# Kernel tuning notes

Hardware: AMD Instinct MI355X
Metric: run time of the kernel (lower is better)

The kernel has to match this reference:

```python
import jax, jax.numpy as jnp
import numpy as np

N_NODES = 50000
N_EDGES = 800000
D_FEAT = 64
K_HOPS = 8


def setup_inputs() -> dict:
    key = jax.random.key(0)
    k1, k2 = jax.random.split(key)
    feature = jax.random.normal(k1, (N_NODES, D_FEAT), dtype=jnp.float32)
    edge_index = jax.random.randint(k2, (2, N_EDGES), 0, N_NODES, dtype=jnp.int32)
    return {"feature": feature, "edge_index": edge_index}


def reference(feature, edge_index):
    # with A_hat = D^{-1/2} (A + I) D^{-1/2} (add_remaining_self_loops + sym_norm).
    n = feature.shape[0]
    src, dst = edge_index[0], edge_index[1]
    # add_remaining_self_loops: drop any existing self-loop edges (weight -> 0)
    # and append a self loop of weight fill_value=1 for every node. Zeroing the
    # weight is mathematically identical to removing the edge.
    ew = jnp.where(src == dst, 0.0, 1.0).astype(feature.dtype)
    loop = jnp.arange(n, dtype=src.dtype)
    row = jnp.concatenate([src, loop])          # message source (x_j)
    col = jnp.concatenate([dst, loop])          # aggregation target (i)
    w = jnp.concatenate([ew, jnp.ones((n,), dtype=feature.dtype)])
    # symmetric normalization: deg over row, norm = d^-1/2[row] * w * d^-1/2[col]
    deg = jax.ops.segment_sum(w, row, num_segments=n)
    deg_inv_sqrt = jnp.where(deg > 0, jax.lax.rsqrt(deg), 0.0)
    norm = deg_inv_sqrt[row] * w * deg_inv_sqrt[col]  # [E+N]

    xs = [feature]
    x = feature
    for _ in range(K_HOPS):  # small fixed K, structural loop
        # gather-scale-scatter_add: out[i] = sum_{(j,i) in E} norm * x[j]
        x = jax.ops.segment_sum(norm[:, None] * x[row], col, num_segments=n)
        xs.append(x)
    return jnp.concatenate(xs, axis=1)  # [N, (K+1)*D]
```

## Files before the change

### kernel.cpp

```cpp
#include <hip/hip_runtime.h>
#include <hip/hip_fp16.h>
#include <hip/hip_fp8.h>

#define N_NODES 50000
#define N_EDGES 800000
#define D_FEAT 64
#define K_HOPS 8
#define OUT_STRIDE ((K_HOPS + 1) * D_FEAT)
#define NPART 128
#define CHUNK (N_EDGES / NPART)
#define NWORD (N_NODES / 2)

#define SCAN_WORDS 512
#define SCAN_NB ((NWORD + SCAN_WORDS - 1) / SCAN_WORDS)

#define NOCT (N_NODES / 8)

#define ALIGN256(x) (((x) + 255) & ~(size_t)255)
static const size_t OFF_P     = 0;
static const size_t OFF_BASES = OFF_P + (size_t)NPART * NWORD * 4;
static const size_t OFF_OFF   = ALIGN256(OFF_BASES + (size_t)NPART * N_NODES * 4);
static const size_t OFF_BSUM  = ALIGN256(OFF_OFF   + (size_t)(N_NODES + 1) * 4);
static const size_t OFF_TOTW  = ALIGN256(OFF_BSUM  + 64 * 4);
static const size_t OFF_DINV  = ALIGN256(OFF_TOTW  + (size_t)NWORD * 4);
static const size_t OFF_CSR   = ALIGN256(OFF_DINV  + (size_t)N_NODES * 4);
static const size_t OFF_XA    = ALIGN256(OFF_CSR   + (size_t)N_EDGES * 4);
static const size_t OFF_XB    = ALIGN256(OFF_XA + (size_t)(N_NODES + 1) * D_FEAT);

__device__ __forceinline__ float2 fp8x2_to_f2(unsigned short s) {
    __hip_fp8x2_e4m3 v;
    v.__x = (__hip_fp8x2_storage_t)s;
    return (float2)v;
}
__device__ __forceinline__ unsigned short f2_to_fp8x2(float a, float b) {
    __hip_fp8x2_e4m3 v(make_float2(a, b));
    return (unsigned short)v.__x;
}
__device__ __forceinline__ unsigned pack_fp8x4(float a, float b, float c, float d) {
    return (unsigned)f2_to_fp8x2(a, b) | ((unsigned)f2_to_fp8x2(c, d) << 16);
}


__global__ __launch_bounds__(256, 1) void k_hist(const int* __restrict__ src,
                                                 const int* __restrict__ dst,
                                                 unsigned* __restrict__ p) {
    __shared__ unsigned h[NWORD];
    int t = threadIdx.x;
    int base = blockIdx.x * CHUNK;
    for (int w = t; w < NWORD; w += 256) h[w] = 0u;
    __syncthreads();
    for (int j = t; j < CHUNK; j += 256) {
        int s = src[base + j], d = dst[base + j];
        if (s != d) {
            atomicAdd(&h[s >> 1], 1u << (8 * (s & 1)));
            atomicAdd(&h[d >> 1], 65536u << (8 * (d & 1)));
        }
    }
    __syncthreads();
    unsigned* o = p + (size_t)blockIdx.x * NWORD;
    for (int w = t; w < NWORD; w += 256) o[w] = h[w];
}

__global__ void k_sum(const unsigned* __restrict__ p, float* __restrict__ dinv,
                      unsigned* __restrict__ totW) {
    int w = blockIdx.x * blockDim.x + threadIdx.x;
    if (w >= NWORD) return;
    unsigned s0 = 0, s1 = 0, s2 = 0, s3 = 0;
    #pragma unroll 4
    for (int c = 0; c < NPART; c += 4) {
        s0 += p[(size_t)(c + 0) * NWORD + w];
        s1 += p[(size_t)(c + 1) * NWORD + w];
        s2 += p[(size_t)(c + 2) * NWORD + w];
        s3 += p[(size_t)(c + 3) * NWORD + w];
    }
    unsigned s = (s0 + s1) + (s2 + s3);
    dinv[2 * w + 0] = rsqrtf((float)((s & 0xffu) + 1u));
    dinv[2 * w + 1] = rsqrtf((float)(((s >> 8) & 0xffu) + 1u));
    totW[w] = ((s >> 16) & 0xffu) | ((s >> 24) << 16);
}

__global__ void k_scan_sums(const unsigned* __restrict__ totW, int* __restrict__ bsum) {
    __shared__ int lds[256];
    int b = blockIdx.x, t = threadIdx.x;
    int wend = min((b + 1) * SCAN_WORDS, NWORD);
    int tot = 0;
    for (int w = b * SCAN_WORDS + t; w < wend; w += 256) {
        unsigned v = totW[w];
        tot += (int)(v & 0xffffu) + (int)(v >> 16);
    }
    lds[t] = tot; __syncthreads();
    for (int str = 128; str > 0; str >>= 1) {
        if (t < str) lds[t] += lds[t + str];
        __syncthreads();
    }
    if (t == 0) bsum[b] = lds[0];
}

__global__ void k_scan_top(int* __restrict__ bsum) {
    int lane = threadIdx.x;
    int orig = (lane < SCAN_NB) ? bsum[lane] : 0;
    int v = orig;
    for (int d = 1; d < 64; d <<= 1) {
        int u = __shfl_up(v, d, 64);
        if (lane >= d) v += u;
    }
    if (lane < SCAN_NB) bsum[lane] = v - orig;
}

__global__ void k_scan_downA(const unsigned* __restrict__ totW, const int* __restrict__ bsum,
                             int* __restrict__ off) {
    __shared__ int lds[256];
    int b = blockIdx.x, t = threadIdx.x;
    int w0 = b * SCAN_WORDS + 2 * t;
    unsigned t0 = (w0 < NWORD) ? totW[w0] : 0u;
    unsigned t1 = (w0 + 1 < NWORD) ? totW[w0 + 1] : 0u;
    int n[4] = { (int)(t0 & 0xffffu), (int)(t0 >> 16),
                 (int)(t1 & 0xffffu), (int)(t1 >> 16) };
    int tsum = (n[0] + n[1]) + (n[2] + n[3]);
    lds[t] = tsum; __syncthreads();
    int x = tsum;
    for (int d = 1; d < 256; d <<= 1) {
        int u = (t >= d) ? lds[t - d] : 0;
        __syncthreads();
        x += u;
        lds[t] = x;
        __syncthreads();
    }
    int pfx = (x - tsum) + bsum[b];
    #pragma unroll
    for (int j = 0; j < 4; ++j) {
        int node = 2 * w0 + j;
        if (node < N_NODES) {
            off[node] = pfx;
            pfx += n[j];
        } else if (node == N_NODES) {
            off[node] = pfx;
        }
    }
}

__global__ void k_bases(const unsigned* __restrict__ p, const int* __restrict__ off,
                        int* __restrict__ bases) {
    int node = blockIdx.x * blockDim.x + threadIdx.x;
    if (node >= N_NODES) return;
    int w = node >> 1;
    int sh = 16 + 8 * (node & 1);
    int acc = off[node];
    for (int c = 0; c < NPART; ++c) {
        bases[(size_t)c * N_NODES + node] = acc;
        acc += (int)((p[(size_t)c * NWORD + w] >> sh) & 0xffu);
    }
}

__global__ __launch_bounds__(256, 1) void k_scatter(const int* __restrict__ src,
                                                    const int* __restrict__ dst,
                                                    const int* __restrict__ bases,
                                                    int* __restrict__ csr) {
    __shared__ unsigned h[NWORD];
    int t = threadIdx.x;
    int base = blockIdx.x * CHUNK;
    const int* bp = bases + (size_t)blockIdx.x * N_NODES;
    for (int w = t; w < NWORD; w += 256) h[w] = 0u;
    __syncthreads();
    for (int j = t; j < CHUNK; j += 256) {
        int s = src[base + j], d = dst[base + j];
        if (s == d) continue;
        unsigned old = atomicAdd(&h[d >> 1], (d & 1) ? 65536u : 1u);
        unsigned pw = (d & 1) ? (old >> 16) : (old & 0xffffu);
        csr[bp[d] + (int)pw] = s;
    }
}


__global__ void k_x0(const float4* __restrict__ feat4, float4* __restrict__ out4,
                     unsigned* __restrict__ y8, const float* __restrict__ dinv) {
    int t = blockIdx.x * blockDim.x + threadIdx.x;
    if (t >= (N_NODES + 1) * 16) return;
    int row = t >> 4;
    if (row < N_NODES) {
        float4 v = feat4[t];
        out4[(size_t)row * (OUT_STRIDE / 4) + (t & 15)] = v;
        float di = dinv[row];
        y8[t] = pack_fp8x4(v.x * di, v.y * di, v.z * di, v.w * di);
    } else {
        y8[t] = 0u;
    }
}

template <bool WRITE_HALF>
__global__ __launch_bounds__(256) void k_hopf8(
    const uint2* __restrict__ yin,
    float4* __restrict__ outcol4,
    uint2* __restrict__ yout,
    const int* __restrict__ off, const int* __restrict__ csr,
    const float* __restrict__ dinv) {
    int ow = (blockIdx.x * blockDim.x + threadIdx.x) >> 6;
    if (ow >= NOCT) return;
    int lane = threadIdx.x & 63;
    int f = lane & 7;
    int node = ow * 8 + (lane >> 3);
    int e0 = off[node], e1 = off[node + 1];
    int deg = e1 - e0;
    float di = dinv[node];
    float a0 = 0.f, a1 = 0.f, a2 = 0.f, a3 = 0.f;
    float a4 = 0.f, a5 = 0.f, a6 = 0.f, a7 = 0.f;
    {
        uint2 sv = yin[(size_t)node * 8 + f];
        float2 u;
        u = fp8x2_to_f2((unsigned short)(sv.x & 0xffffu)); a0 = u.x; a1 = u.y;
        u = fp8x2_to_f2((unsigned short)(sv.x >> 16));     a2 = u.x; a3 = u.y;
        u = fp8x2_to_f2((unsigned short)(sv.y & 0xffffu)); a4 = u.x; a5 = u.y;
        u = fp8x2_to_f2((unsigned short)(sv.y >> 16));     a6 = u.x; a7 = u.y;
    }

    int nm = deg;
    #pragma unroll
    for (int d = 32; d; d >>= 1) nm = max(nm, __shfl_xor(nm, d, 64));

    int gbase = lane & ~7;

    #define ACC8(q)                                                        \
        {                                                                  \
            float2 u_;                                                     \
            u_ = fp8x2_to_f2((unsigned short)((q).x & 0xffffu));           \
            a0 += u_.x; a1 += u_.y;                                        \
            u_ = fp8x2_to_f2((unsigned short)((q).x >> 16));               \
            a2 += u_.x; a3 += u_.y;                                        \
            u_ = fp8x2_to_f2((unsigned short)((q).y & 0xffffu));           \
            a4 += u_.x; a5 += u_.y;                                        \
            u_ = fp8x2_to_f2((unsigned short)((q).y >> 16));               \
            a6 += u_.x; a7 += u_.y;                                        \
        }

    int cvec = csr[min(e0 + f, N_EDGES - 1)];
    for (int j = 0; j < nm; j += 8) {
        int cnext = csr[min(e0 + j + 8 + f, N_EDGES - 1)];
        int v0 = (j + 0 < deg) ? __shfl(cvec, gbase + 0, 64) : N_NODES;
        int v1 = (j + 1 < deg) ? __shfl(cvec, gbase + 1, 64) : N_NODES;
        int v2 = (j + 2 < deg) ? __shfl(cvec, gbase + 2, 64) : N_NODES;
        int v3 = (j + 3 < deg) ? __shfl(cvec, gbase + 3, 64) : N_NODES;
        int v4 = (j + 4 < deg) ? __shfl(cvec, gbase + 4, 64) : N_NODES;
        int v5 = (j + 5 < deg) ? __shfl(cvec, gbase + 5, 64) : N_NODES;
        int v6 = (j + 6 < deg) ? __shfl(cvec, gbase + 6, 64) : N_NODES;
        int v7 = (j + 7 < deg) ? __shfl(cvec, gbase + 7, 64) : N_NODES;
        uint2 q0 = yin[(size_t)v0 * 8 + f];
        uint2 q1 = yin[(size_t)v1 * 8 + f];
        uint2 q2 = yin[(size_t)v2 * 8 + f];
        uint2 q3 = yin[(size_t)v3 * 8 + f];
        uint2 q4 = yin[(size_t)v4 * 8 + f];
        uint2 q5 = yin[(size_t)v5 * 8 + f];
        uint2 q6 = yin[(size_t)v6 * 8 + f];
        uint2 q7 = yin[(size_t)v7 * 8 + f];
        ACC8(q0) ACC8(q1) ACC8(q2) ACC8(q3)
        ACC8(q4) ACC8(q5) ACC8(q6) ACC8(q7)
        cvec = cnext;
    }
    #undef ACC8

    size_t orow = (size_t)node * (OUT_STRIDE / 4) + 2 * f;
    outcol4[orow]     = make_float4(di * a0, di * a1, di * a2, di * a3);
    outcol4[orow + 1] = make_float4(di * a4, di * a5, di * a6, di * a7);
    if (WRITE_HALF) {
        float di2 = di * di;
        uint2 w;
        w.x = pack_fp8x4(di2 * a0, di2 * a1, di2 * a2, di2 * a3);
        w.y = pack_fp8x4(di2 * a4, di2 * a5, di2 * a6, di2 * a7);
        yout[(size_t)node * 8 + f] = w;
        if (blockIdx.x == 0 && threadIdx.x < 8)
            yout[(size_t)N_NODES * 8 + threadIdx.x] = make_uint2(0u, 0u);
    }
}


extern "C" void kernel_launch(void* const* d_in, const int* in_sizes, int n_in,
                              void* d_out, int out_size, void* d_ws, size_t ws_size,
                              hipStream_t stream) {
    const float* feature = (const float*)d_in[0];
    const int* edge = (const int*)d_in[1];
    const int* src = edge;
    const int* dst = edge + N_EDGES;
    float* out = (float*)d_out;
    char* ws = (char*)d_ws;

    unsigned* p     = (unsigned*)(ws + OFF_P);
    int*      bases = (int*)(ws + OFF_BASES);
    int*      off   = (int*)(ws + OFF_OFF);
    int*      bsum  = (int*)(ws + OFF_BSUM);
    unsigned* totW  = (unsigned*)(ws + OFF_TOTW);
    float*    dinv  = (float*)(ws + OFF_DINV);
    int*      csr   = (int*)(ws + OFF_CSR);
    uint2*    xa    = (uint2*)(ws + OFF_XA);
    uint2*    xb    = (uint2*)(ws + OFF_XB);

    const int TB = 256;
    const int NB_NODES = (N_NODES + TB - 1) / TB;
    k_hist<<<NPART, 256, 0, stream>>>(src, dst, p);
    k_sum<<<(NWORD + TB - 1) / TB, TB, 0, stream>>>(p, dinv, totW);
    k_x0<<<((N_NODES + 1) * 16 + TB - 1) / TB, TB, 0, stream>>>(
        (const float4*)feature, (float4*)out, (unsigned*)xb, dinv);
    k_scan_sums<<<SCAN_NB, 256, 0, stream>>>(totW, bsum);
    k_scan_top<<<1, 64, 0, stream>>>(bsum);
    k_scan_downA<<<SCAN_NB, 256, 0, stream>>>(totW, bsum, off);
    k_bases<<<NB_NODES, TB, 0, stream>>>(p, off, bases);
    k_scatter<<<NPART, 256, 0, stream>>>(src, dst, bases, csr);
    const int hop_blocks = (NOCT * 64 + TB - 1) / TB;
    for (int k = 1; k <= K_HOPS; ++k) {
        const uint2* yin = (k & 1) ? xb : xa;
        uint2* yout      = (k & 1) ? xa : xb;
        float4* outcol4 = (float4*)out + (size_t)k * 16;
        if (k < K_HOPS)
            k_hopf8<true><<<hop_blocks, TB, 0, stream>>>(yin, outcol4, yout, off, csr, dinv);
        else
            k_hopf8<false><<<hop_blocks, TB, 0, stream>>>(yin, outcol4, nullptr, off, csr, dinv);
    }
}
```

Measured before the change: 296.9 us.

## Sort nodes by degree so hop wavefronts process similar-degree nodes

Adds a counting-sort pass (histogram, scan, placement) that builds a permutation of nodes in descending degree order, capped at 63. Each hop kernel then maps its 8 nodes per wavefront through this permutation. The aim is to cut load imbalance, since each wave loops to the maximum degree among its nodes. In exchange it adds three small kernels, one extra indirection per node, and less locality for the output-row writes and the y reads/writes, which are now scattered by node.

```diff
diff --git a/kernel.cpp b/kernel.cpp
--- a/kernel.cpp
+++ b/kernel.cpp
@@ -16,6 +16,9 @@
 
 #define NOCT (N_NODES / 8)
 
+#define DNB 50
+#define DCHUNK (N_NODES / DNB)
+
 #define ALIGN256(x) (((x) + 255) & ~(size_t)255)
 static const size_t OFF_P     = 0;
 static const size_t OFF_BASES = OFF_P + (size_t)NPART * NWORD * 4;
@@ -24,7 +27,10 @@
 static const size_t OFF_TOTW  = ALIGN256(OFF_BSUM  + 64 * 4);
 static const size_t OFF_DINV  = ALIGN256(OFF_TOTW  + (size_t)NWORD * 4);
 static const size_t OFF_CSR   = ALIGN256(OFF_DINV  + (size_t)N_NODES * 4);
-static const size_t OFF_XA    = ALIGN256(OFF_CSR   + (size_t)N_EDGES * 4);
+static const size_t OFF_DPART = ALIGN256(OFF_CSR   + (size_t)N_EDGES * 4);
+static const size_t OFF_DBASE = ALIGN256(OFF_DPART + DNB * 64 * 4);
+static const size_t OFF_PERM  = ALIGN256(OFF_DBASE + DNB * 64 * 4);
+static const size_t OFF_XA    = ALIGN256(OFF_PERM  + (size_t)N_NODES * 4);
 static const size_t OFF_XB    = ALIGN256(OFF_XA + (size_t)(N_NODES + 1) * D_FEAT);
 
 __device__ __forceinline__ float2 fp8x2_to_f2(unsigned short s) {
@@ -172,6 +178,65 @@
 }
 
 
+__global__ void k_dhist(const int* __restrict__ off, int* __restrict__ dpart) {
+    __shared__ int h[64];
+    int t = threadIdx.x;
+    if (t < 64) h[t] = 0;
+    __syncthreads();
+    int base = blockIdx.x * DCHUNK;
+    for (int j = t; j < DCHUNK; j += 256) {
+        int deg = off[base + j + 1] - off[base + j];
+        atomicAdd(&h[63 - min(deg, 63)], 1);
+    }
+    __syncthreads();
+    if (t < 64) dpart[blockIdx.x * 64 + t] = h[t];
+}
+
+__global__ void k_dscan(const int* __restrict__ dpart, int* __restrict__ dbase) {
+    __shared__ int colsum[64];
+    __shared__ int binstart[64];
+    int t = threadIdx.x;
+    if (t < 64) {
+        int s = 0;
+        for (int b = 0; b < DNB; ++b) s += dpart[b * 64 + t];
+        colsum[t] = s;
+    }
+    __syncthreads();
+    if (t < 64) {
+        int v = colsum[t], x = v;
+        for (int d = 1; d < 64; d <<= 1) {
+            int u = __shfl_up(x, d, 64);
+            if (t >= d) x += u;
+        }
+        binstart[t] = x - v;
+    }
+    __syncthreads();
+    if (t < 64) {
+        int acc = binstart[t];
+        for (int b = 0; b < DNB; ++b) {
+            dbase[b * 64 + t] = acc;
+            acc += dpart[b * 64 + t];
+        }
+    }
+}
+
+__global__ void k_dplace(const int* __restrict__ off, const int* __restrict__ dbase,
+                         int* __restrict__ perm) {
+    __shared__ int h[64];
+    int t = threadIdx.x;
+    if (t < 64) h[t] = 0;
+    __syncthreads();
+    int base = blockIdx.x * DCHUNK;
+    const int* db = dbase + blockIdx.x * 64;
+    for (int j = t; j < DCHUNK; j += 256) {
+        int node = base + j;
+        int bin = 63 - min(off[node + 1] - off[node], 63);
+        int slot = atomicAdd(&h[bin], 1);
+        perm[db[bin] + slot] = node;
+    }
+}
+
+
 __global__ void k_x0(const float4* __restrict__ feat4, float4* __restrict__ out4,
                      unsigned* __restrict__ y8, const float* __restrict__ dinv) {
     int t = blockIdx.x * blockDim.x + threadIdx.x;
@@ -193,12 +258,12 @@
     float4* __restrict__ outcol4,
     uint2* __restrict__ yout,
     const int* __restrict__ off, const int* __restrict__ csr,
-    const float* __restrict__ dinv) {
+    const float* __restrict__ dinv, const int* __restrict__ perm) {
     int ow = (blockIdx.x * blockDim.x + threadIdx.x) >> 6;
     if (ow >= NOCT) return;
     int lane = threadIdx.x & 63;
     int f = lane & 7;
-    int node = ow * 8 + (lane >> 3);
+    int node = perm[ow * 8 + (lane >> 3)];
     int e0 = off[node], e1 = off[node + 1];
     int deg = e1 - e0;
     float di = dinv[node];
@@ -289,6 +354,9 @@
     unsigned* totW  = (unsigned*)(ws + OFF_TOTW);
     float*    dinv  = (float*)(ws + OFF_DINV);
     int*      csr   = (int*)(ws + OFF_CSR);
+    int*      dpart = (int*)(ws + OFF_DPART);
+    int*      dbase = (int*)(ws + OFF_DBASE);
+    int*      perm  = (int*)(ws + OFF_PERM);
     uint2*    xa    = (uint2*)(ws + OFF_XA);
     uint2*    xb    = (uint2*)(ws + OFF_XB);
 
@@ -301,6 +369,9 @@
     k_scan_sums<<<SCAN_NB, 256, 0, stream>>>(totW, bsum);
     k_scan_top<<<1, 64, 0, stream>>>(bsum);
     k_scan_downA<<<SCAN_NB, 256, 0, stream>>>(totW, bsum, off);
+    k_dhist<<<DNB, 256, 0, stream>>>(off, dpart);
+    k_dscan<<<1, 256, 0, stream>>>(dpart, dbase);
+    k_dplace<<<DNB, 256, 0, stream>>>(off, dbase, perm);
     k_bases<<<NB_NODES, TB, 0, stream>>>(p, off, bases);
     k_scatter<<<NPART, 256, 0, stream>>>(src, dst, bases, csr);
     const int hop_blocks = (NOCT * 64 + TB - 1) / TB;
@@ -309,8 +380,8 @@
         uint2* yout      = (k & 1) ? xa : xb;
         float4* outcol4 = (float4*)out + (size_t)k * 16;
         if (k < K_HOPS)
-            k_hopf8<true><<<hop_blocks, TB, 0, stream>>>(yin, outcol4, yout, off, csr, dinv);
+            k_hopf8<true><<<hop_blocks, TB, 0, stream>>>(yin, outcol4, yout, off, csr, dinv, perm);
         else
-            k_hopf8<false><<<hop_blocks, TB, 0, stream>>>(yin, outcol4, nullptr, off, csr, dinv);
-    }
-}
+            k_hopf8<false><<<hop_blocks, TB, 0, stream>>>(yin, outcol4, nullptr, off, csr, dinv, perm);
+    }
+}
```

New measurement: 305.0 us. 1.03x slower.
